# Kernel tuning notes

Hardware: AMD Instinct MI355X
Metric: run time of the kernel (lower is better)

## Reference

```python
import jax, jax.numpy as jnp
import numpy as np

B, NQ, S, E, H = 8, 200, 4096, 2048, 8  # batch, total queries, kv len, embed dim, heads


def setup_inputs() -> dict:
    key = jax.random.key(0)
    ks = jax.random.split(key, 8)
    s = 0.02
    return {
        "q": jax.random.normal(ks[0], (B, NQ, E), dtype=jnp.float32),
        "k": jax.random.normal(ks[1], (B, S, E), dtype=jnp.float32),
        "v": jax.random.normal(ks[2], (B, S, E), dtype=jnp.float32),
        # Linear weights stored as [in, out] so y = x @ W + b (math-equivalent to torch x @ W.T + b)
        "wq": jax.random.normal(ks[3], (E, E), dtype=jnp.float32) * s,
        "bq": jnp.zeros((E,), jnp.float32),
        "wk": jax.random.normal(ks[4], (E, E), dtype=jnp.float32) * s,
        "bk": jnp.zeros((E,), jnp.float32),
        "wv": jax.random.normal(ks[5], (E, E), dtype=jnp.float32) * s,
        "bv": jnp.zeros((E,), jnp.float32),
        "wo": jax.random.normal(ks[6], (E, E), dtype=jnp.float32) * s,
        "bo": jnp.zeros((E,), jnp.float32),
        "tau": jnp.ones((), jnp.float32),
        "n": 100,
    }


def _split_heads(x, h):
    b, t, c = x.shape
    return x.reshape(b, t, h, c // h).transpose(0, 2, 1, 3)  # [b,h,t,c/h]


def reference(q, k, v, wq, bq, wk, bk, wv, bv, wo, bo, tau, n):
    qp = q @ wq + bq
    kp = k @ wk + bk
    vp = v @ wv + bv

    q1 = qp[:, :n]  # gumbel branch queries
    q2 = qp[:, n:]  # standard branch queries
    q1 = q1 / jnp.linalg.norm(q1, axis=-1, keepdims=True)
    k1 = kp / jnp.linalg.norm(kp, axis=-1, keepdims=True)

    q1h = _split_heads(q1, H)
    q2h = _split_heads(q2, H)
    kh = _split_heads(kp, H)
    k1h = _split_heads(k1, H)
    vh = _split_heads(vp, H)
    c_per_head = q1h.shape[-1]

    # Branch 1: cosine-similarity scores -> hard gumbel-softmax over the QUERY axis (-2)
    attn1 = jnp.einsum('bhqc,bhkc->bhqk', q1h, k1h)
    # Branch 2: scaled dot-product softmax over key axis
    attn2 = jnp.einsum('bhqc,bhkc->bhqk', q2h, kh) / jnp.sqrt(jnp.float32(c_per_head))
    attn2 = jax.nn.softmax(attn2, axis=-1)

    # gumbel_softmax(hard=True, dim=-2): deterministic fixed-key gumbel noise
    u = jax.random.uniform(jax.random.key(42), attn1.shape, minval=1e-6, maxval=1.0 - 1e-6)
    g = -jnp.log(-jnp.log(u))
    soft = jax.nn.softmax((attn1 + g) / tau, axis=-2)
    idx = jnp.argmax(soft, axis=-2)  # [b,h,kv]
    hard = jnp.moveaxis(jax.nn.one_hot(idx, n, dtype=soft.dtype), -1, -2)  # [b,h,n,kv]
    attn1 = hard - jax.lax.stop_gradient(soft) + soft  # straight-through

    # dropout p=0.0 -> identity
    out1 = jnp.einsum('bhqk,bhkc->bhqc', attn1, vh)
    out2 = jnp.einsum('bhqk,bhkc->bhqc', attn2, vh)
    out = jnp.concatenate([out1, out2], axis=2)  # concat along token axis
    out = out.transpose(0, 2, 1, 3).reshape(out.shape[0], out.shape[2], -1)  # recombine heads
    return out @ wo + bo
```

## Files before the change

### kernel.cpp

```cpp
#include <hip/hip_runtime.h>

#define B_   8
#define NQ_  200
#define S_   4096
#define E_   2048
#define H_   8
#define CH_  256
#define NN_  100

typedef short v8s  __attribute__((ext_vector_type(8)));
typedef float v4f  __attribute__((ext_vector_type(4)));

__device__ __forceinline__ unsigned rotl32(unsigned x, int d) {
    return (x << d) | (x >> (32 - d));
}

__device__ __forceinline__ unsigned threefry_bits(unsigned x0, unsigned x1) {
    const unsigned ks0 = 0u;
    const unsigned ks1 = 42u;
    const unsigned ks2 = 0x1BD11BDAu ^ 0u ^ 42u;
    x0 += ks0; x1 += ks1;
#define TFR(d) { x0 += x1; x1 = rotl32(x1, d); x1 ^= x0; }
    TFR(13) TFR(15) TFR(26) TFR(6)
    x0 += ks1; x1 += ks2 + 1u;
    TFR(17) TFR(29) TFR(16) TFR(24)
    x0 += ks2; x1 += ks0 + 2u;
    TFR(13) TFR(15) TFR(26) TFR(6)
    x0 += ks0; x1 += ks1 + 3u;
    TFR(17) TFR(29) TFR(16) TFR(24)
    x0 += ks1; x1 += ks2 + 4u;
    TFR(13) TFR(15) TFR(26) TFR(6)
    x0 += ks2; x1 += ks0 + 5u;
#undef TFR
    return x0 ^ x1;
}

__device__ __forceinline__ double gumbel_from_index(unsigned i) {
    unsigned bits = threefry_bits(0u, i);
    float f = __uint_as_float((bits >> 9) | 0x3F800000u) - 1.0f;
    const float minv = 1e-6f;
    const float maxv = (float)(1.0 - 1e-6);
    float span = __fsub_rn(maxv, minv);
    float u = __fadd_rn(__fmul_rn(f, span), minv);
    u = fmaxf(minv, u);
    double lg = log((double)u);
    return -log(-lg);
}

__device__ __forceinline__ unsigned short f2bf(float f) {
    unsigned u = __float_as_uint(f);
    unsigned r = (u + 0x7FFFu + ((u >> 16) & 1u)) >> 16;
    return (unsigned short)r;
}

__device__ __forceinline__ float bf2f(unsigned short h) {
    return __uint_as_float(((unsigned)h) << 16);
}

#define ASYNC16(g, l)                                                          \
    __builtin_amdgcn_global_load_lds(                                          \
        (const __attribute__((address_space(1))) unsigned*)(g),                \
        (__attribute__((address_space(3))) unsigned*)(l), 16, 0, 0)

template <bool TB, bool BIAS>
__global__ __launch_bounds__(256)
void gemm_f32(const float* __restrict__ A, const float* __restrict__ Bm,
              const float* __restrict__ bias, float* __restrict__ C,
              int M, int N, int K, int lda, int ldb, int ldc,
              long saO, long saI, long sbO, long sbI, long scO, long scI)
{
    const int z  = blockIdx.z;
    const int zo = z >> 3, zi = z & 7;
    A  += (long)zo * saO + (long)zi * saI;
    Bm += (long)zo * sbO + (long)zi * sbI;
    C  += (long)zo * scO + (long)zi * scI;

    const int tid = threadIdx.x;
    const int n0  = blockIdx.x * 128;
    const int m0  = blockIdx.y * 128;

    __shared__ float As[16][132];
    __shared__ float Bs[16][132];

    float acc[8][8] = {};

    const int tx = tid & 15, ty = tid >> 4;

    for (int k0 = 0; k0 < K; k0 += 16) {
        {
            const int kk = (tid & 3) * 4;
#pragma unroll
            for (int p = 0; p < 2; ++p) {
                const int mi = (tid >> 2) + p * 64;
                const int m  = m0 + mi;
                float4 v = make_float4(0.f, 0.f, 0.f, 0.f);
                if (m < M) v = *(const float4*)(A + (long)m * lda + k0 + kk);
                As[kk + 0][mi] = v.x; As[kk + 1][mi] = v.y;
                As[kk + 2][mi] = v.z; As[kk + 3][mi] = v.w;
            }
        }
        if (TB) {
            const int kk = (tid & 3) * 4;
#pragma unroll
            for (int p = 0; p < 2; ++p) {
                const int ni = (tid >> 2) + p * 64;
                const int nn = n0 + ni;
                float4 v = make_float4(0.f, 0.f, 0.f, 0.f);
                if (nn < N) v = *(const float4*)(Bm + (long)nn * ldb + k0 + kk);
                Bs[kk + 0][ni] = v.x; Bs[kk + 1][ni] = v.y;
                Bs[kk + 2][ni] = v.z; Bs[kk + 3][ni] = v.w;
            }
        } else {
#pragma unroll
            for (int p = 0; p < 2; ++p) {
                const int kk = (tid >> 5) + p * 8;
                const int ni = (tid & 31) * 4;
                float4 v = *(const float4*)(Bm + (long)(k0 + kk) * ldb + n0 + ni);
                *(float4*)&Bs[kk][ni] = v;
            }
        }
        __syncthreads();

#pragma unroll
        for (int kk = 0; kk < 16; ++kk) {
            float a[8], b[8];
            *(float4*)&a[0] = *(const float4*)&As[kk][ty * 4];
            *(float4*)&a[4] = *(const float4*)&As[kk][64 + ty * 4];
            *(float4*)&b[0] = *(const float4*)&Bs[kk][tx * 4];
            *(float4*)&b[4] = *(const float4*)&Bs[kk][64 + tx * 4];
#pragma unroll
            for (int i = 0; i < 8; ++i)
#pragma unroll
                for (int j = 0; j < 8; ++j)
                    acc[i][j] += a[i] * b[j];
        }
        __syncthreads();
    }

    float bj[8] = {};
    if (BIAS) {
#pragma unroll
        for (int j = 0; j < 4; ++j) bj[j]     = bias[n0 + tx * 4 + j];
#pragma unroll
        for (int j = 0; j < 4; ++j) bj[4 + j] = bias[n0 + 64 + tx * 4 + j];
    }
#pragma unroll
    for (int i = 0; i < 8; ++i) {
        const int m = m0 + (i < 4 ? ty * 4 + i : 64 + ty * 4 + (i - 4));
        if (m >= M) continue;
        float4 o0, o1;
        o0.x = acc[i][0] + bj[0]; o0.y = acc[i][1] + bj[1];
        o0.z = acc[i][2] + bj[2]; o0.w = acc[i][3] + bj[3];
        o1.x = acc[i][4] + bj[4]; o1.y = acc[i][5] + bj[5];
        o1.z = acc[i][6] + bj[6]; o1.w = acc[i][7] + bj[7];
        float* cp = C + (long)m * ldc + n0;
        *(float4*)(cp + tx * 4)      = o0;
        *(float4*)(cp + 64 + tx * 4) = o1;
    }
}

template <bool BIAS>
__global__ __launch_bounds__(256)
void gemm_bf16_bt(const unsigned short* __restrict__ A,
                  const unsigned short* __restrict__ Bt,
                  const float* __restrict__ bias,
                  float* __restrict__ C,
                  int M, int N, int K)
{
    __shared__ unsigned short Asm[128 * 32];
    __shared__ unsigned short Bsm[128 * 32];

    const int tid  = threadIdx.x;
    const int lane = tid & 63;
    const int wave = tid >> 6;
    const int m0 = blockIdx.y * 128;
    const int n0 = blockIdx.x * 128;

    const int woffm = (wave & 1) * 64;
    const int woffn = (wave >> 1) * 64;
    const int mrow = lane & 15;
    const int quad = lane >> 4;
    const int ko   = quad * 8;

    v4f acc[4][4] = {};

    const long  arow0 = (long)(m0 + (tid >> 2)) * K + (tid & 3) * 8;
    const long  arow1 = (long)(m0 + 64 + (tid >> 2)) * K + (tid & 3) * 8;
    const long  brow0 = (long)(n0 + (tid >> 2)) * K + (tid & 3) * 8;
    const long  brow1 = (long)(n0 + 64 + (tid >> 2)) * K + (tid & 3) * 8;

    for (int k0 = 0; k0 < K; k0 += 32) {
        ASYNC16(A + arow0 + k0,  &Asm[tid * 8]);
        ASYNC16(A + arow1 + k0,  &Asm[(256 + tid) * 8]);
        ASYNC16(Bt + brow0 + k0, &Bsm[tid * 8]);
        ASYNC16(Bt + brow1 + k0, &Bsm[(256 + tid) * 8]);
        __syncthreads();

        v8s a[4], b[4];
#pragma unroll
        for (int i = 0; i < 4; ++i)
            a[i] = *(const v8s*)&Asm[(woffm + i * 16 + mrow) * 32 + ko];
#pragma unroll
        for (int j = 0; j < 4; ++j)
            b[j] = *(const v8s*)&Bsm[(woffn + j * 16 + mrow) * 32 + ko];
#pragma unroll
        for (int i = 0; i < 4; ++i)
#pragma unroll
            for (int j = 0; j < 4; ++j)
                acc[i][j] = __builtin_amdgcn_mfma_f32_16x16x32_bf16(
                    a[i], b[j], acc[i][j], 0, 0, 0);
        __syncthreads();
    }

    const int col = mrow;
    const int r0  = quad * 4;
#pragma unroll
    for (int j = 0; j < 4; ++j) {
        const int n = n0 + woffn + j * 16 + col;
        const float bv = BIAS ? bias[n] : 0.f;
#pragma unroll
        for (int i = 0; i < 4; ++i) {
            const int mbase = m0 + woffm + i * 16 + r0;
#pragma unroll
            for (int r = 0; r < 4; ++r) {
                const int m = mbase + r;
                if (m < M) C[(long)m * N + n] = acc[i][j][r] + bv;
            }
        }
    }
}

template <bool BIAS>
__global__ __launch_bounds__(256)
void gemm_bf16x3_bt(const unsigned short* __restrict__ Ahi,
                    const unsigned short* __restrict__ Alo,
                    const unsigned short* __restrict__ Bhi,
                    const unsigned short* __restrict__ Blo,
                    const float* __restrict__ bias,
                    float* __restrict__ C,
                    int M, int N, int K)
{
    __shared__ unsigned short AsmH[128 * 32];
    __shared__ unsigned short AsmL[128 * 32];
    __shared__ unsigned short BsmH[128 * 32];
    __shared__ unsigned short BsmL[128 * 32];

    const int tid  = threadIdx.x;
    const int lane = tid & 63;
    const int wave = tid >> 6;
    const int m0 = blockIdx.y * 128;
    const int n0 = blockIdx.x * 128;

    const int woffm = (wave & 1) * 64;
    const int woffn = (wave >> 1) * 64;
    const int mrow = lane & 15;
    const int quad = lane >> 4;
    const int ko   = quad * 8;

    v4f acc[4][4] = {};

    const long  arow0 = (long)(m0 + (tid >> 2)) * K + (tid & 3) * 8;
    const long  arow1 = (long)(m0 + 64 + (tid >> 2)) * K + (tid & 3) * 8;
    const long  brow0 = (long)(n0 + (tid >> 2)) * K + (tid & 3) * 8;
    const long  brow1 = (long)(n0 + 64 + (tid >> 2)) * K + (tid & 3) * 8;

    for (int k0 = 0; k0 < K; k0 += 32) {
        ASYNC16(Ahi + arow0 + k0, &AsmH[tid * 8]);
        ASYNC16(Ahi + arow1 + k0, &AsmH[(256 + tid) * 8]);
        ASYNC16(Alo + arow0 + k0, &AsmL[tid * 8]);
        ASYNC16(Alo + arow1 + k0, &AsmL[(256 + tid) * 8]);
        ASYNC16(Bhi + brow0 + k0, &BsmH[tid * 8]);
        ASYNC16(Bhi + brow1 + k0, &BsmH[(256 + tid) * 8]);
        ASYNC16(Blo + brow0 + k0, &BsmL[tid * 8]);
        ASYNC16(Blo + brow1 + k0, &BsmL[(256 + tid) * 8]);
        __syncthreads();

        v8s ah[4], al[4], bh[4], bl[4];
#pragma unroll
        for (int i = 0; i < 4; ++i) {
            const int off = (woffm + i * 16 + mrow) * 32 + ko;
            ah[i] = *(const v8s*)&AsmH[off];
            al[i] = *(const v8s*)&AsmL[off];
        }
#pragma unroll
        for (int j = 0; j < 4; ++j) {
            const int off = (woffn + j * 16 + mrow) * 32 + ko;
            bh[j] = *(const v8s*)&BsmH[off];
            bl[j] = *(const v8s*)&BsmL[off];
        }
#pragma unroll
        for (int i = 0; i < 4; ++i)
#pragma unroll
            for (int j = 0; j < 4; ++j) {
                acc[i][j] = __builtin_amdgcn_mfma_f32_16x16x32_bf16(
                    ah[i], bh[j], acc[i][j], 0, 0, 0);
                acc[i][j] = __builtin_amdgcn_mfma_f32_16x16x32_bf16(
                    ah[i], bl[j], acc[i][j], 0, 0, 0);
                acc[i][j] = __builtin_amdgcn_mfma_f32_16x16x32_bf16(
                    al[i], bh[j], acc[i][j], 0, 0, 0);
            }
        __syncthreads();
    }

    const int col = mrow;
    const int r0  = quad * 4;
#pragma unroll
    for (int j = 0; j < 4; ++j) {
        const int n = n0 + woffn + j * 16 + col;
        const float bv = BIAS ? bias[n] : 0.f;
#pragma unroll
        for (int i = 0; i < 4; ++i) {
            const int mbase = m0 + woffm + i * 16 + r0;
#pragma unroll
            for (int r = 0; r < 4; ++r) {
                const int m = mbase + r;
                if (m < M) C[(long)m * N + n] = acc[i][j][r] + bv;
            }
        }
    }
}

__global__ __launch_bounds__(256)
void cast_f32_bf16(const float* __restrict__ in, unsigned short* __restrict__ out, long n)
{
    long i = ((long)blockIdx.x * 256 + threadIdx.x) * 8;
    if (i + 8 <= n) {
        float4 v0 = *(const float4*)(in + i);
        float4 v1 = *(const float4*)(in + i + 4);
        ushort4 a, b;
        a.x = f2bf(v0.x); a.y = f2bf(v0.y); a.z = f2bf(v0.z); a.w = f2bf(v0.w);
        b.x = f2bf(v1.x); b.y = f2bf(v1.y); b.z = f2bf(v1.z); b.w = f2bf(v1.w);
        *(ushort4*)(out + i)     = a;
        *(ushort4*)(out + i + 4) = b;
    } else {
        for (; i < n; ++i) out[i] = f2bf(in[i]);
    }
}

__global__ __launch_bounds__(256)
void split_cast_hi_lo(const float* __restrict__ in,
                      unsigned short* __restrict__ hi,
                      unsigned short* __restrict__ lo, long n)
{
    long i = ((long)blockIdx.x * 256 + threadIdx.x) * 8;
    if (i + 8 <= n) {
        float4 v0 = *(const float4*)(in + i);
        float4 v1 = *(const float4*)(in + i + 4);
        float x[8] = {v0.x, v0.y, v0.z, v0.w, v1.x, v1.y, v1.z, v1.w};
        unsigned short h[8], l[8];
#pragma unroll
        for (int j = 0; j < 8; ++j) {
            unsigned short hb = f2bf(x[j]);
            h[j] = hb;
            l[j] = f2bf(x[j] - bf2f(hb));
        }
        *(ushort4*)(hi + i)     = make_ushort4(h[0], h[1], h[2], h[3]);
        *(ushort4*)(hi + i + 4) = make_ushort4(h[4], h[5], h[6], h[7]);
        *(ushort4*)(lo + i)     = make_ushort4(l[0], l[1], l[2], l[3]);
        *(ushort4*)(lo + i + 4) = make_ushort4(l[4], l[5], l[6], l[7]);
    } else {
        for (; i < n; ++i) {
            unsigned short hb = f2bf(in[i]);
            hi[i] = hb;
            lo[i] = f2bf(in[i] - bf2f(hb));
        }
    }
}

__global__ __launch_bounds__(256)
void transpose_cast(const float* __restrict__ W, unsigned short* __restrict__ Wt,
                    int Kd, int Nd)
{
    __shared__ float t[32][33];
    const int nb = blockIdx.x * 32, kb = blockIdx.y * 32;
    const int tx = threadIdx.x & 31, ty = threadIdx.x >> 5;
#pragma unroll
    for (int p = 0; p < 4; ++p)
        t[ty + p * 8][tx] = W[(long)(kb + ty + p * 8) * Nd + nb + tx];
    __syncthreads();
#pragma unroll
    for (int p = 0; p < 4; ++p)
        Wt[(long)(nb + ty + p * 8) * Kd + kb + tx] = f2bf(t[tx][ty + p * 8]);
}

__global__ __launch_bounds__(256)
void transpose_split_cast(const float* __restrict__ W,
                          unsigned short* __restrict__ WtHi,
                          unsigned short* __restrict__ WtLo,
                          int Kd, int Nd)
{
    __shared__ float t[32][33];
    const int nb = blockIdx.x * 32, kb = blockIdx.y * 32;
    const int tx = threadIdx.x & 31, ty = threadIdx.x >> 5;
#pragma unroll
    for (int p = 0; p < 4; ++p)
        t[ty + p * 8][tx] = W[(long)(kb + ty + p * 8) * Nd + nb + tx];
    __syncthreads();
#pragma unroll
    for (int p = 0; p < 4; ++p) {
        float x = t[tx][ty + p * 8];
        unsigned short hb = f2bf(x);
        long idx = (long)(nb + ty + p * 8) * Kd + kb + tx;
        WtHi[idx] = hb;
        WtLo[idx] = f2bf(x - bf2f(hb));
    }
}

__global__ __launch_bounds__(256)
void row_invnorm(const float* __restrict__ src, double* __restrict__ out,
                 int perBatch, long batchStride)
{
    const int r = blockIdx.x;
    const int b = r / perBatch, i = r % perBatch;
    const float* row = src + (long)b * batchStride + (long)i * E_;
    double s = 0.0;
    for (int c = threadIdx.x; c < E_; c += 256) {
        float v = row[c];
        s += (double)v * (double)v;
    }
    for (int off = 32; off; off >>= 1) s += __shfl_down(s, off, 64);
    __shared__ double wred[4];
    if ((threadIdx.x & 63) == 0) wred[threadIdx.x >> 6] = s;
    __syncthreads();
    if (threadIdx.x == 0)
        out[r] = 1.0 / sqrt(wred[0] + wred[1] + wred[2] + wred[3]);
}

__global__ __launch_bounds__(256)
void gumbel_argmax_scatter_v2(const float* __restrict__ S1,
                              const float* __restrict__ vp,
                              const double* __restrict__ invqn,
                              const double* __restrict__ invkn,
                              const float* __restrict__ taup,
                              float* __restrict__ outcat)
{
    const int h   = blockIdx.y;
    const int b   = blockIdx.z;
    const int tid = threadIdx.x;
    const int k0  = blockIdx.x * 256;
    const int k   = k0 + tid;

    __shared__ double iqs[NN_];
    __shared__ int    idxs[256];

    for (int e = tid; e < NN_; e += 256) iqs[e] = invqn[b * NN_ + e];
    __syncthreads();

    const double itau = 1.0 / (double)taup[0];
    const double ikd  = invkn[b * S_ + k];
    const float* sp   = S1 + (long)(b * H_ + h) * NN_ * S_ + k;
    const unsigned ibase = (unsigned)((b * H_ + h) * NN_) * (unsigned)S_ + (unsigned)k;

    double best = -1e300;
    int bi = 0;
#pragma unroll 1
    for (int q = 0; q < NN_; ++q) {
        const double g  = gumbel_from_index(ibase + (unsigned)q * (unsigned)S_);
        const double zv = ((double)sp[(long)q * S_] * (iqs[q] * ikd) + g) * itau;
        if (zv > best) { best = zv; bi = q; }
    }
    idxs[tid] = bi;
    __syncthreads();

    for (int kk = 0; kk < 256; ++kk) {
        const int row = idxs[kk];
        const float v = vp[((long)b * S_ + (k0 + kk)) * E_ + h * CH_ + tid];
        atomicAdd(outcat + ((long)b * NQ_ + row) * E_ + h * CH_ + tid, v);
    }
}

__global__ __launch_bounds__(256)
void softmax_rows(float* __restrict__ S2)
{
    const long r = blockIdx.x;
    float* row = S2 + r * (long)S_;
    __shared__ float buf[S_];
    __shared__ float wred[4];
    __shared__ float wsum[4];
    const int tid = threadIdx.x;

    float mx = -1e30f;
    for (int c = tid; c < S_; c += 256) {
        float v = row[c];
        buf[c] = v;
        mx = fmaxf(mx, v);
    }
    for (int off = 32; off; off >>= 1) mx = fmaxf(mx, __shfl_xor(mx, off, 64));
    if ((tid & 63) == 0) wred[tid >> 6] = mx;
    __syncthreads();
    mx = fmaxf(fmaxf(wred[0], wred[1]), fmaxf(wred[2], wred[3]));

    float sum = 0.f;
    for (int c = tid; c < S_; c += 256) {
        float p = __expf((buf[c] - mx) * 0.0625f);
        buf[c] = p;
        sum += p;
    }
    for (int off = 32; off; off >>= 1) sum += __shfl_xor(sum, off, 64);
    if ((tid & 63) == 0) wsum[tid >> 6] = sum;
    __syncthreads();
    sum = wsum[0] + wsum[1] + wsum[2] + wsum[3];
    const float inv = 1.0f / sum;
    for (int c = tid; c < S_; c += 256) row[c] = buf[c] * inv;
}

extern "C" void kernel_launch(void* const* d_in, const int* in_sizes, int n_in,
                              void* d_out, int out_size, void* d_ws, size_t ws_size,
                              hipStream_t stream)
{
    const float* q   = (const float*)d_in[0];
    const float* k   = (const float*)d_in[1];
    const float* v   = (const float*)d_in[2];
    const float* wq  = (const float*)d_in[3];
    const float* bq  = (const float*)d_in[4];
    const float* wk  = (const float*)d_in[5];
    const float* bk  = (const float*)d_in[6];
    const float* wv  = (const float*)d_in[7];
    const float* bv  = (const float*)d_in[8];
    const float* wo  = (const float*)d_in[9];
    const float* bo  = (const float*)d_in[10];
    const float* tau = (const float*)d_in[11];

    char* ws = (char*)d_ws;
    float*          qp       = (float*)(ws + 0L);
    float*          kp       = (float*)(ws + 13107200L);
    float*          vp       = (float*)(ws + 281542656L);
    unsigned short* k_hi     = (unsigned short*)(ws + 281542656L);
    unsigned short* k_lo     = (unsigned short*)(ws + 415760384L);
    float*          outcat   = (float*)(ws + 549978112L);
    float*          S2       = (float*)(ws + 563085312L);
    float*          S1       = (float*)(ws + 563085312L);
    unsigned short* wkThi    = (unsigned short*)(ws + 563085312L);
    unsigned short* wkTlo    = (unsigned short*)(ws + 571473920L);
    unsigned short* v_bf16c  = (unsigned short*)(ws + 563085312L);
    unsigned short* wT1      = (unsigned short*)(ws + 630194176L);
    unsigned short* out_bf16 = (unsigned short*)(ws + 563085312L);
    unsigned short* wT2      = (unsigned short*)(ws + 569901056L);
    double*         iqn      = (double*)(ws + 667942912L);
    double*         ikn      = (double*)(ws + 667949312L);

    const dim3 blk(256);

    transpose_split_cast<<<dim3(64, 64), blk, 0, stream>>>(wk, wkThi, wkTlo, 2048, 2048);
    split_cast_hi_lo<<<dim3(32768), blk, 0, stream>>>(k, k_hi, k_lo, (long)32768 * 2048);
    gemm_bf16x3_bt<true><<<dim3(16, 256), blk, 0, stream>>>(
        k_hi, k_lo, wkThi, wkTlo, bk, kp, 32768, 2048, 2048);

    gemm_f32<false, true><<<dim3(16, 13, 1), blk, 0, stream>>>(
        q, wq, bq, qp, 1600, 2048, 2048, 2048, 2048, 2048, 0, 0, 0, 0, 0, 0);

    transpose_cast<<<dim3(64, 64), blk, 0, stream>>>(wv, wT1, 2048, 2048);
    for (int c = 0; c < 2; ++c) {
        cast_f32_bf16<<<dim3(16384), blk, 0, stream>>>(
            v + (long)c * 16384 * 2048, v_bf16c, (long)16384 * 2048);
        gemm_bf16_bt<true><<<dim3(16, 128), blk, 0, stream>>>(
            v_bf16c, wT1, bv, vp + (long)c * 16384 * 2048, 16384, 2048, 2048);
    }

    row_invnorm<<<dim3(800), blk, 0, stream>>>(qp, iqn, NN_, (long)NQ_ * E_);
    row_invnorm<<<dim3(32768), blk, 0, stream>>>(kp, ikn, S_, (long)S_ * E_);
    gemm_f32<true, false><<<dim3(32, 1, 64), blk, 0, stream>>>(
        qp, kp, nullptr, S1,
        100, 4096, 256, 2048, 2048, 4096,
        (long)NQ_ * E_, (long)CH_,
        (long)S_ * E_, (long)CH_,
        (long)H_ * NN_ * S_, (long)NN_ * S_);
    hipMemsetAsync(outcat, 0, 13107200, stream);
    gumbel_argmax_scatter_v2<<<dim3(16, 8, 8), blk, 0, stream>>>(
        S1, vp, iqn, ikn, tau, outcat);

    gemm_f32<true, false><<<dim3(32, 1, 64), blk, 0, stream>>>(
        qp + (long)NN_ * E_, kp, nullptr, S2,
        100, 4096, 256, 2048, 2048, 4096,
        (long)NQ_ * E_, (long)CH_,
        (long)S_ * E_, (long)CH_,
        (long)H_ * NN_ * S_, (long)NN_ * S_);
    softmax_rows<<<dim3(6400), blk, 0, stream>>>(S2);
    gemm_f32<false, false><<<dim3(2, 1, 64), blk, 0, stream>>>(
        S2, vp, nullptr, outcat + (long)NN_ * E_,
        100, 256, 4096, 4096, 2048, 2048,
        (long)H_ * NN_ * S_, (long)NN_ * S_,
        (long)S_ * E_, (long)CH_,
        (long)NQ_ * E_, (long)CH_);

    cast_f32_bf16<<<dim3(1600), blk, 0, stream>>>(outcat, out_bf16, (long)1600 * 2048);
    transpose_cast<<<dim3(64, 64), blk, 0, stream>>>(wo, wT2, 2048, 2048);
    gemm_bf16_bt<true><<<dim3(16, 13), blk, 0, stream>>>(
        out_bf16, wT2, bo, (float*)d_out, 1600, 2048, 2048);
}
```

Measured before the change: 3.849 ms.

## Use bf16x3 MFMA for attention scores, split-K PV, LDS-accumulated gumbel scatter

The K projection now writes its output directly as bf16 hi/lo pairs, and the Q projection is split the same way. A new bf16x3 MFMA kernel computes both attention score matrices, replacing the fp32 SIMT GEMM. The gumbel scatter now accumulates V rows per query in LDS over 1024 keys before issuing one atomic per output element, instead of one atomic per key. The PV GEMM is split four ways along K and combined with atomicAdd. The bf16 GEMMs also gain an XCD-aware block swizzle and clamp their row loads. These changes aim to cut fp32 GEMM cost, global atomic traffic and cross-XCD cache misses. In exchange they add atomics and a very large LDS footprint in the scatter kernel, and the three-product bf16 split may change precision slightly.

```diff
diff --git a/kernel.cpp b/kernel.cpp
--- a/kernel.cpp
+++ b/kernel.cpp
@@ -62,17 +62,30 @@
         (const __attribute__((address_space(1))) unsigned*)(g),                \
         (__attribute__((address_space(3))) unsigned*)(l), 16, 0, 0)
 
-template <bool TB, bool BIAS>
+__device__ __forceinline__ void xcd_swizzle(int& bx, int& by) {
+    const int nwg = gridDim.x * gridDim.y;
+    int flat = blockIdx.y * gridDim.x + blockIdx.x;
+    if ((nwg & 7) == 0) {
+        const int cpx = nwg >> 3;
+        flat = (flat & 7) * cpx + (flat >> 3);
+    }
+    bx = flat % gridDim.x;
+    by = flat / gridDim.x;
+}
+
+template <bool TB, bool BIAS, bool ATOMIC>
 __global__ __launch_bounds__(256)
 void gemm_f32(const float* __restrict__ A, const float* __restrict__ Bm,
               const float* __restrict__ bias, float* __restrict__ C,
               int M, int N, int K, int lda, int ldb, int ldc,
               long saO, long saI, long sbO, long sbI, long scO, long scI)
 {
-    const int z  = blockIdx.z;
+    const int zc = blockIdx.z;
+    const int kc = zc >> 6;
+    const int z  = zc & 63;
     const int zo = z >> 3, zi = z & 7;
-    A  += (long)zo * saO + (long)zi * saI;
-    Bm += (long)zo * sbO + (long)zi * sbI;
+    A  += (long)zo * saO + (long)zi * saI + (long)kc * K;
+    Bm += (long)zo * sbO + (long)zi * sbI + (TB ? (long)kc * K : (long)kc * K * ldb);
     C  += (long)zo * scO + (long)zi * scI;
 
     const int tid = threadIdx.x;
@@ -148,14 +161,21 @@
     for (int i = 0; i < 8; ++i) {
         const int m = m0 + (i < 4 ? ty * 4 + i : 64 + ty * 4 + (i - 4));
         if (m >= M) continue;
-        float4 o0, o1;
-        o0.x = acc[i][0] + bj[0]; o0.y = acc[i][1] + bj[1];
-        o0.z = acc[i][2] + bj[2]; o0.w = acc[i][3] + bj[3];
-        o1.x = acc[i][4] + bj[4]; o1.y = acc[i][5] + bj[5];
-        o1.z = acc[i][6] + bj[6]; o1.w = acc[i][7] + bj[7];
         float* cp = C + (long)m * ldc + n0;
-        *(float4*)(cp + tx * 4)      = o0;
-        *(float4*)(cp + 64 + tx * 4) = o1;
+        if (ATOMIC) {
+#pragma unroll
+            for (int j = 0; j < 4; ++j) atomicAdd(cp + tx * 4 + j,      acc[i][j]);
+#pragma unroll
+            for (int j = 0; j < 4; ++j) atomicAdd(cp + 64 + tx * 4 + j, acc[i][4 + j]);
+        } else {
+            float4 o0, o1;
+            o0.x = acc[i][0] + bj[0]; o0.y = acc[i][1] + bj[1];
+            o0.z = acc[i][2] + bj[2]; o0.w = acc[i][3] + bj[3];
+            o1.x = acc[i][4] + bj[4]; o1.y = acc[i][5] + bj[5];
+            o1.z = acc[i][6] + bj[6]; o1.w = acc[i][7] + bj[7];
+            *(float4*)(cp + tx * 4)      = o0;
+            *(float4*)(cp + 64 + tx * 4) = o1;
+        }
     }
 }
 
@@ -170,11 +190,14 @@
     __shared__ unsigned short Asm[128 * 32];
     __shared__ unsigned short Bsm[128 * 32];
 
+    int bx, by;
+    xcd_swizzle(bx, by);
+
     const int tid  = threadIdx.x;
     const int lane = tid & 63;
     const int wave = tid >> 6;
-    const int m0 = blockIdx.y * 128;
-    const int n0 = blockIdx.x * 128;
+    const int m0 = by * 128;
+    const int n0 = bx * 128;
 
     const int woffm = (wave & 1) * 64;
     const int woffn = (wave >> 1) * 64;
@@ -184,8 +207,10 @@
 
     v4f acc[4][4] = {};
 
-    const long  arow0 = (long)(m0 + (tid >> 2)) * K + (tid & 3) * 8;
-    const long  arow1 = (long)(m0 + 64 + (tid >> 2)) * K + (tid & 3) * 8;
+    const int ar0 = min(m0 + (tid >> 2), M - 1);
+    const int ar1 = min(m0 + 64 + (tid >> 2), M - 1);
+    const long  arow0 = (long)ar0 * K + (tid & 3) * 8;
+    const long  arow1 = (long)ar1 * K + (tid & 3) * 8;
     const long  brow0 = (long)(n0 + (tid >> 2)) * K + (tid & 3) * 8;
     const long  brow1 = (long)(n0 + 64 + (tid >> 2)) * K + (tid & 3) * 8;
 
@@ -230,7 +255,7 @@
     }
 }
 
-template <bool BIAS>
+template <bool BIAS, bool SPLITOUT>
 __global__ __launch_bounds__(256)
 void gemm_bf16x3_bt(const unsigned short* __restrict__ Ahi,
                     const unsigned short* __restrict__ Alo,
@@ -238,6 +263,8 @@
                     const unsigned short* __restrict__ Blo,
                     const float* __restrict__ bias,
                     float* __restrict__ C,
+                    unsigned short* __restrict__ Chi,
+                    unsigned short* __restrict__ Clo,
                     int M, int N, int K)
 {
     __shared__ unsigned short AsmH[128 * 32];
@@ -245,11 +272,14 @@
     __shared__ unsigned short BsmH[128 * 32];
     __shared__ unsigned short BsmL[128 * 32];
 
+    int bx, by;
+    xcd_swizzle(bx, by);
+
     const int tid  = threadIdx.x;
     const int lane = tid & 63;
     const int wave = tid >> 6;
-    const int m0 = blockIdx.y * 128;
-    const int n0 = blockIdx.x * 128;
+    const int m0 = by * 128;
+    const int n0 = bx * 128;
 
     const int woffm = (wave & 1) * 64;
     const int woffn = (wave >> 1) * 64;
@@ -259,8 +289,10 @@
 
     v4f acc[4][4] = {};
 
-    const long  arow0 = (long)(m0 + (tid >> 2)) * K + (tid & 3) * 8;
-    const long  arow1 = (long)(m0 + 64 + (tid >> 2)) * K + (tid & 3) * 8;
+    const int ar0 = min(m0 + (tid >> 2), M - 1);
+    const int ar1 = min(m0 + 64 + (tid >> 2), M - 1);
+    const long  arow0 = (long)ar0 * K + (tid & 3) * 8;
+    const long  arow1 = (long)ar1 * K + (tid & 3) * 8;
     const long  brow0 = (long)(n0 + (tid >> 2)) * K + (tid & 3) * 8;
     const long  brow1 = (long)(n0 + 64 + (tid >> 2)) * K + (tid & 3) * 8;
 
@@ -314,7 +346,107 @@
 #pragma unroll
             for (int r = 0; r < 4; ++r) {
                 const int m = mbase + r;
-                if (m < M) C[(long)m * N + n] = acc[i][j][r] + bv;
+                if (m < M) {
+                    const float o = acc[i][j][r] + bv;
+                    if (SPLITOUT) {
+                        const unsigned short hb = f2bf(o);
+                        Chi[(long)m * N + n] = hb;
+                        Clo[(long)m * N + n] = f2bf(o - bf2f(hb));
+                    } else {
+                        C[(long)m * N + n] = o;
+                    }
+                }
+            }
+        }
+    }
+}
+
+__global__ __launch_bounds__(256)
+void attn_scores_bf16x3(const unsigned short* __restrict__ Qhi,
+                        const unsigned short* __restrict__ Qlo,
+                        const unsigned short* __restrict__ Khi,
+                        const unsigned short* __restrict__ Klo,
+                        float* __restrict__ Sout, int qRowOff)
+{
+    __shared__ unsigned short AsmH[128 * 32];
+    __shared__ unsigned short AsmL[128 * 32];
+    __shared__ unsigned short BsmH[128 * 32];
+    __shared__ unsigned short BsmL[128 * 32];
+
+    const int z = blockIdx.z;
+    const int b = z >> 3, h = z & 7;
+    const int n0 = blockIdx.x * 128;
+
+    const int tid  = threadIdx.x;
+    const int lane = tid & 63;
+    const int wave = tid >> 6;
+
+    const int woffm = (wave & 1) * 64;
+    const int woffn = (wave >> 1) * 64;
+    const int mrow = lane & 15;
+    const int quad = lane >> 4;
+    const int ko   = quad * 8;
+
+    v4f acc[4][4] = {};
+
+    const int ar0 = min(b * NQ_ + qRowOff + (tid >> 2), B_ * NQ_ - 1);
+    const int ar1 = min(b * NQ_ + qRowOff + 64 + (tid >> 2), B_ * NQ_ - 1);
+    const long abase0 = (long)ar0 * E_ + h * CH_ + (tid & 3) * 8;
+    const long abase1 = (long)ar1 * E_ + h * CH_ + (tid & 3) * 8;
+    const long bbase0 = (long)((long)b * S_ + n0 + (tid >> 2)) * E_ + h * CH_ + (tid & 3) * 8;
+    const long bbase1 = (long)((long)b * S_ + n0 + 64 + (tid >> 2)) * E_ + h * CH_ + (tid & 3) * 8;
+
+    for (int k0 = 0; k0 < CH_; k0 += 32) {
+        ASYNC16(Qhi + abase0 + k0, &AsmH[tid * 8]);
+        ASYNC16(Qhi + abase1 + k0, &AsmH[(256 + tid) * 8]);
+        ASYNC16(Qlo + abase0 + k0, &AsmL[tid * 8]);
+        ASYNC16(Qlo + abase1 + k0, &AsmL[(256 + tid) * 8]);
+        ASYNC16(Khi + bbase0 + k0, &BsmH[tid * 8]);
+        ASYNC16(Khi + bbase1 + k0, &BsmH[(256 + tid) * 8]);
+        ASYNC16(Klo + bbase0 + k0, &BsmL[tid * 8]);
+        ASYNC16(Klo + bbase1 + k0, &BsmL[(256 + tid) * 8]);
+        __syncthreads();
+
+        v8s ah[4], al[4], bh[4], bl[4];
+#pragma unroll
+        for (int i = 0; i < 4; ++i) {
+            const int off = (woffm + i * 16 + mrow) * 32 + ko;
+            ah[i] = *(const v8s*)&AsmH[off];
+            al[i] = *(const v8s*)&AsmL[off];
+        }
+#pragma unroll
+        for (int j = 0; j < 4; ++j) {
+            const int off = (woffn + j * 16 + mrow) * 32 + ko;
+            bh[j] = *(const v8s*)&BsmH[off];
+            bl[j] = *(const v8s*)&BsmL[off];
+        }
+#pragma unroll
+        for (int i = 0; i < 4; ++i)
+#pragma unroll
+            for (int j = 0; j < 4; ++j) {
+                acc[i][j] = __builtin_amdgcn_mfma_f32_16x16x32_bf16(
+                    ah[i], bh[j], acc[i][j], 0, 0, 0);
+                acc[i][j] = __builtin_amdgcn_mfma_f32_16x16x32_bf16(
+                    ah[i], bl[j], acc[i][j], 0, 0, 0);
+                acc[i][j] = __builtin_amdgcn_mfma_f32_16x16x32_bf16(
+                    al[i], bh[j], acc[i][j], 0, 0, 0);
+            }
+        __syncthreads();
+    }
+
+    float* Cb = Sout + (long)z * NN_ * S_;
+    const int col = mrow;
+    const int r0  = quad * 4;
+#pragma unroll
+    for (int j = 0; j < 4; ++j) {
+        const int n = n0 + woffn + j * 16 + col;
+#pragma unroll
+        for (int i = 0; i < 4; ++i) {
+            const int mbase = woffm + i * 16 + r0;
+#pragma unroll
+            for (int r = 0; r < 4; ++r) {
+                const int m = mbase + r;
+                if (m < NN_) Cb[(long)m * S_ + n] = acc[i][j][r];
             }
         }
     }
@@ -427,46 +559,79 @@
 }
 
 __global__ __launch_bounds__(256)
-void gumbel_argmax_scatter_v2(const float* __restrict__ S1,
+void row_invnorm_hl(const unsigned short* __restrict__ hi,
+                    const unsigned short* __restrict__ lo,
+                    double* __restrict__ out)
+{
+    const long r = blockIdx.x;
+    const long base = r * E_ + (long)threadIdx.x * 8;
+    v8s vh = *(const v8s*)(hi + base);
+    v8s vl = *(const v8s*)(lo + base);
+    double s = 0.0;
+#pragma unroll
+    for (int j = 0; j < 8; ++j) {
+        float v = bf2f((unsigned short)vh[j]) + bf2f((unsigned short)vl[j]);
+        s += (double)v * (double)v;
+    }
+    for (int off = 32; off; off >>= 1) s += __shfl_down(s, off, 64);
+    __shared__ double wred[4];
+    if ((threadIdx.x & 63) == 0) wred[threadIdx.x >> 6] = s;
+    __syncthreads();
+    if (threadIdx.x == 0)
+        out[r] = 1.0 / sqrt(wred[0] + wred[1] + wred[2] + wred[3]);
+}
+
+__global__ __launch_bounds__(256)
+void gumbel_argmax_scatter_v3(const float* __restrict__ S1,
                               const float* __restrict__ vp,
                               const double* __restrict__ invqn,
                               const double* __restrict__ invkn,
                               const float* __restrict__ taup,
                               float* __restrict__ outcat)
 {
+    const int kc  = blockIdx.x;
     const int h   = blockIdx.y;
     const int b   = blockIdx.z;
     const int tid = threadIdx.x;
-    const int k0  = blockIdx.x * 256;
-    const int k   = k0 + tid;
-
+    const int k0  = kc * 1024;
+
+    __shared__ float  accum[NN_][256];
+    __shared__ int    idxs[1024];
     __shared__ double iqs[NN_];
-    __shared__ int    idxs[256];
 
     for (int e = tid; e < NN_; e += 256) iqs[e] = invqn[b * NN_ + e];
+#pragma unroll
+    for (int r = tid; r < NN_ * 256; r += 256) ((float*)accum)[r] = 0.f;
     __syncthreads();
 
     const double itau = 1.0 / (double)taup[0];
-    const double ikd  = invkn[b * S_ + k];
-    const float* sp   = S1 + (long)(b * H_ + h) * NN_ * S_ + k;
-    const unsigned ibase = (unsigned)((b * H_ + h) * NN_) * (unsigned)S_ + (unsigned)k;
-
-    double best = -1e300;
-    int bi = 0;
+    const float* S1b = S1 + (long)(b * H_ + h) * NN_ * S_;
+
+    for (int p = 0; p < 4; ++p) {
+        const int k = k0 + p * 256 + tid;
+        const double ikd = invkn[b * S_ + k];
+        const unsigned ibase = (unsigned)((b * H_ + h) * NN_) * (unsigned)S_ + (unsigned)k;
+        double best = -1e300;
+        int bi = 0;
 #pragma unroll 1
-    for (int q = 0; q < NN_; ++q) {
-        const double g  = gumbel_from_index(ibase + (unsigned)q * (unsigned)S_);
-        const double zv = ((double)sp[(long)q * S_] * (iqs[q] * ikd) + g) * itau;
-        if (zv > best) { best = zv; bi = q; }
-    }
-    idxs[tid] = bi;
-    __syncthreads();
-
-    for (int kk = 0; kk < 256; ++kk) {
-        const int row = idxs[kk];
-        const float v = vp[((long)b * S_ + (k0 + kk)) * E_ + h * CH_ + tid];
-        atomicAdd(outcat + ((long)b * NQ_ + row) * E_ + h * CH_ + tid, v);
-    }
+        for (int q = 0; q < NN_; ++q) {
+            const double g  = gumbel_from_index(ibase + (unsigned)q * (unsigned)S_);
+            const double zv = ((double)S1b[(long)q * S_ + k] * (iqs[q] * ikd) + g) * itau;
+            if (zv > best) { best = zv; bi = q; }
+        }
+        idxs[p * 256 + tid] = bi;
+    }
+    __syncthreads();
+
+    const float* vrow = vp + ((long)b * S_ + k0) * E_ + h * CH_ + tid;
+#pragma unroll 4
+    for (int kk = 0; kk < 1024; ++kk) {
+        accum[idxs[kk]][tid] += vrow[(long)kk * E_];
+    }
+    __syncthreads();
+
+    for (int q = 0; q < NN_; ++q)
+        atomicAdd(outcat + ((long)b * NQ_ + q) * E_ + h * CH_ + tid, accum[q][tid]);
 }
 
 __global__ __launch_bounds__(256)
@@ -522,14 +687,16 @@
     const float* tau = (const float*)d_in[11];
 
     char* ws = (char*)d_ws;
-    float*          qp       = (float*)(ws + 0L);
-    float*          kp       = (float*)(ws + 13107200L);
+    unsigned short* qp_hi    = (unsigned short*)(ws + 0L);
+    unsigned short* qp_lo    = (unsigned short*)(ws + 6553600L);
+    unsigned short* kp_hi    = (unsigned short*)(ws + 13107200L);
+    unsigned short* kp_lo    = (unsigned short*)(ws + 147324928L);
     float*          vp       = (float*)(ws + 281542656L);
     unsigned short* k_hi     = (unsigned short*)(ws + 281542656L);
     unsigned short* k_lo     = (unsigned short*)(ws + 415760384L);
     float*          outcat   = (float*)(ws + 549978112L);
-    float*          S2       = (float*)(ws + 563085312L);
-    float*          S1       = (float*)(ws + 563085312L);
+    float*          qpf      = (float*)(ws + 549978112L);
+    float*          Sreg     = (float*)(ws + 563085312L);
     unsigned short* wkThi    = (unsigned short*)(ws + 563085312L);
     unsigned short* wkTlo    = (unsigned short*)(ws + 571473920L);
     unsigned short* v_bf16c  = (unsigned short*)(ws + 563085312L);
@@ -543,11 +710,13 @@
 
     transpose_split_cast<<<dim3(64, 64), blk, 0, stream>>>(wk, wkThi, wkTlo, 2048, 2048);
     split_cast_hi_lo<<<dim3(32768), blk, 0, stream>>>(k, k_hi, k_lo, (long)32768 * 2048);
-    gemm_bf16x3_bt<true><<<dim3(16, 256), blk, 0, stream>>>(
-        k_hi, k_lo, wkThi, wkTlo, bk, kp, 32768, 2048, 2048);
-
-    gemm_f32<false, true><<<dim3(16, 13, 1), blk, 0, stream>>>(
-        q, wq, bq, qp, 1600, 2048, 2048, 2048, 2048, 2048, 0, 0, 0, 0, 0, 0);
+    gemm_bf16x3_bt<true, true><<<dim3(16, 256), blk, 0, stream>>>(
+        k_hi, k_lo, wkThi, wkTlo, bk, nullptr, kp_hi, kp_lo, 32768, 2048, 2048);
+
+    gemm_f32<false, true, false><<<dim3(16, 13, 1), blk, 0, stream>>>(
+        q, wq, bq, qpf, 1600, 2048, 2048, 2048, 2048, 2048, 0, 0, 0, 0, 0, 0);
+    row_invnorm<<<dim3(800), blk, 0, stream>>>(qpf, iqn, NN_, (long)NQ_ * E_);
+    split_cast_hi_lo<<<dim3(1600), blk, 0, stream>>>(qpf, qp_hi, qp_lo, (long)1600 * 2048);
 
     transpose_cast<<<dim3(64, 64), blk, 0, stream>>>(wv, wT1, 2048, 2048);
     for (int c = 0; c < 2; ++c) {
@@ -557,28 +726,20 @@
             v_bf16c, wT1, bv, vp + (long)c * 16384 * 2048, 16384, 2048, 2048);
     }
 
-    row_invnorm<<<dim3(800), blk, 0, stream>>>(qp, iqn, NN_, (long)NQ_ * E_);
-    row_invnorm<<<dim3(32768), blk, 0, stream>>>(kp, ikn, S_, (long)S_ * E_);
-    gemm_f32<true, false><<<dim3(32, 1, 64), blk, 0, stream>>>(
-        qp, kp, nullptr, S1,
-        100, 4096, 256, 2048, 2048, 4096,
-        (long)NQ_ * E_, (long)CH_,
-        (long)S_ * E_, (long)CH_,
-        (long)H_ * NN_ * S_, (long)NN_ * S_);
+    row_invnorm_hl<<<dim3(32768), blk, 0, stream>>>(kp_hi, kp_lo, ikn);
+
+    attn_scores_bf16x3<<<dim3(32, 1, 64), blk, 0, stream>>>(
+        qp_hi, qp_lo, kp_hi, kp_lo, Sreg, 0);
     hipMemsetAsync(outcat, 0, 13107200, stream);
-    gumbel_argmax_scatter_v2<<<dim3(16, 8, 8), blk, 0, stream>>>(
-        S1, vp, iqn, ikn, tau, outcat);
-
-    gemm_f32<true, false><<<dim3(32, 1, 64), blk, 0, stream>>>(
-        qp + (long)NN_ * E_, kp, nullptr, S2,
-        100, 4096, 256, 2048, 2048, 4096,
-        (long)NQ_ * E_, (long)CH_,
-        (long)S_ * E_, (long)CH_,
-        (long)H_ * NN_ * S_, (long)NN_ * S_);
-    softmax_rows<<<dim3(6400), blk, 0, stream>>>(S2);
-    gemm_f32<false, false><<<dim3(2, 1, 64), blk, 0, stream>>>(
-        S2, vp, nullptr, outcat + (long)NN_ * E_,
-        100, 256, 4096, 4096, 2048, 2048,
+    gumbel_argmax_scatter_v3<<<dim3(4, 8, 8), blk, 0, stream>>>(
+        Sreg, vp, iqn, ikn, tau, outcat);
+
+    attn_scores_bf16x3<<<dim3(32, 1, 64), blk, 0, stream>>>(
+        qp_hi, qp_lo, kp_hi, kp_lo, Sreg, NN_);
+    softmax_rows<<<dim3(6400), blk, 0, stream>>>(Sreg);
+    gemm_f32<false, false, true><<<dim3(2, 1, 256), blk, 0, stream>>>(
+        Sreg, vp, nullptr, outcat + (long)NN_ * E_,
+        100, 256, 1024, 4096, 2048, 2048,
         (long)H_ * NN_ * S_, (long)NN_ * S_,
         (long)S_ * E_, (long)CH_,
         (long)NQ_ * E_, (long)CH_);
```

New measurement: 3.392 ms. 1.13x faster.
